# Optimization experiments

Hardware: AMD Instinct MI355X
Metric: run time of the kernel (lower is better)

## Reference

```python
import jax, jax.numpy as jnp
import numpy as np

EPS = 1e-5

def layer_norm(x, g, b):
    m = jnp.mean(x, axis=-1, keepdims=True)
    v = jnp.var(x, axis=-1, keepdims=True)
    return (x - m) / jnp.sqrt(v + EPS) * g + b

def setup_inputs() -> dict:
    key = jax.random.key(0)
    B, N, D, H, F = 2, 2048, 1024, 16, 4096
    ks = jax.random.split(key, 12)
    s = 0.02
    return {
        "x": jax.random.normal(ks[0], (B, N, D), dtype=jnp.float32),
        "wq": jax.random.normal(ks[1], (D, D), dtype=jnp.float32) * s,
        "bq": jnp.zeros((D,), jnp.float32),
        "wk": jax.random.normal(ks[2], (D, D), dtype=jnp.float32) * s,
        "bk": jnp.zeros((D,), jnp.float32),
        "wv": jax.random.normal(ks[3], (D, D), dtype=jnp.float32) * s,
        "bv": jnp.zeros((D,), jnp.float32),
        "g1": jnp.ones((D,), jnp.float32),
        "b1": jnp.zeros((D,), jnp.float32),
        "g2": jnp.ones((D,), jnp.float32),
        "b2": jnp.zeros((D,), jnp.float32),
        "w1": jax.random.normal(ks[4], (D, F), dtype=jnp.float32) * s,
        "bw1": jnp.zeros((F,), jnp.float32),
        "gf": jnp.ones((F,), jnp.float32),
        "bf": jnp.zeros((F,), jnp.float32),
        "w2": jax.random.normal(ks[5], (F, D), dtype=jnp.float32) * s,
        "bw2": jnp.zeros((D,), jnp.float32),
        "num_heads": 16,
    }

def reference(x, wq, bq, wk, bk, wv, bv, g1, b1, g2, b2, w1, bw1, gf, bf, w2, bw2, num_heads):
    B, N, D = x.shape
    H = num_heads
    E = D // H
    h = layer_norm(x, g1, b1)
    q = (h @ wq + bq).reshape(B, N, H, E).transpose(0, 2, 1, 3)  # B H N E
    k = (h @ wk + bk).reshape(B, N, H, E).transpose(0, 2, 1, 3)
    v = (h @ wv + bv).reshape(B, N, H, E).transpose(0, 2, 1, 3)
    # NOTE: original scales by 1/sqrt(1/emb_dim) == sqrt(emb_dim)
    scale = jnp.sqrt(jnp.float32(D))
    score = jnp.einsum('bhne,bhme->bhnm', q, k) * scale  # B H N N
    w = jax.nn.softmax(score, axis=-1)
    attn = jnp.einsum('bhnm,bhme->bhne', w, v)
    attn = attn.transpose(0, 2, 1, 3).reshape(B, N, D)
    x = x + attn  # dropout = identity in eval
    h2 = layer_norm(x, g2, b2)
    # MLP: Linear -> (Dropout) -> LayerNorm -> ReLU -> Linear; NO residual add (faithful to source)
    u = layer_norm(h2 @ w1 + bw1, gf, bf)
    return jax.nn.relu(u) @ w2 + bw2
```

## Files before the change

kernel.cpp:

```cpp
#include <hip/hip_runtime.h>

typedef unsigned short u16;
typedef _Float16 f16;
typedef _Float16 f16x8 __attribute__((ext_vector_type(8)));
typedef float f32x4 __attribute__((ext_vector_type(4)));
typedef unsigned short u16x4 __attribute__((ext_vector_type(4)));
typedef unsigned int u32x4 __attribute__((ext_vector_type(4)));

__device__ __forceinline__ u16 f2h(float f) {
    f16 h = (f16)f;
    return *reinterpret_cast<u16*>(&h);
}
__device__ __forceinline__ float h2f(u16 u) {
    f16 h = *reinterpret_cast<f16*>(&u);
    return (float)h;
}

__device__ __forceinline__ unsigned cvtpkh(float lo, float hi) {
    unsigned r;
    asm volatile("v_cvt_pkrtz_f16_f32 %0, %1, %2" : "=v"(r) : "v"(lo), "v"(hi));
    return r;
}

__device__ __forceinline__ void gload16(const u16* g, u16* l) {
    __builtin_amdgcn_global_load_lds((const __attribute__((address_space(1))) unsigned int*)g,
                                     (__attribute__((address_space(3))) unsigned int*)l, 16, 0, 0);
}

__global__ void transpose_cast3(const float* __restrict__ W0, u16* __restrict__ T0,
                                const float* __restrict__ W1, u16* __restrict__ T1,
                                const float* __restrict__ W2, u16* __restrict__ T2,
                                int K, int N) {
    __shared__ float t[32][33];
    const float* W = (blockIdx.z == 0) ? W0 : (blockIdx.z == 1) ? W1 : W2;
    u16* Wt = (blockIdx.z == 0) ? T0 : (blockIdx.z == 1) ? T1 : T2;
    const int n0 = blockIdx.x * 32, k0 = blockIdx.y * 32;
    const int tx = threadIdx.x, ty = threadIdx.y;
#pragma unroll
    for (int i = 0; i < 32; i += 8)
        t[ty + i][tx] = W[(size_t)(k0 + ty + i) * N + n0 + tx];
    __syncthreads();
#pragma unroll
    for (int i = 0; i < 32; i += 8)
        Wt[(size_t)(n0 + ty + i) * K + k0 + tx] = f2h(t[tx][ty + i]);
}

__global__ void transpose_cast(const float* __restrict__ W, u16* __restrict__ Wt,
                               int K, int N) {
    __shared__ float t[32][33];
    const int n0 = blockIdx.x * 32, k0 = blockIdx.y * 32;
    const int tx = threadIdx.x, ty = threadIdx.y;
#pragma unroll
    for (int i = 0; i < 32; i += 8)
        t[ty + i][tx] = W[(size_t)(k0 + ty + i) * N + n0 + tx];
    __syncthreads();
#pragma unroll
    for (int i = 0; i < 32; i += 8)
        Wt[(size_t)(n0 + ty + i) * K + k0 + tx] = f2h(t[tx][ty + i]);
}

__global__ __launch_bounds__(256) void ln_f32_f16(const float* __restrict__ in,
                                                  const float* __restrict__ g,
                                                  const float* __restrict__ b,
                                                  u16* __restrict__ out) {
    constexpr int Dl = 1024;
    const int row = blockIdx.x, tid = threadIdx.x;
    const float4 v = *(const float4*)&in[(size_t)row * Dl + tid * 4];
    const float* vp = (const float*)&v;
    float s = v.x + v.y + v.z + v.w;
    float s2 = v.x * v.x + v.y * v.y + v.z * v.z + v.w * v.w;
#pragma unroll
    for (int off = 32; off; off >>= 1) { s += __shfl_xor(s, off); s2 += __shfl_xor(s2, off); }
    __shared__ float red[8];
    const int lane = tid & 63, wid = tid >> 6;
    if (lane == 0) { red[wid] = s; red[4 + wid] = s2; }
    __syncthreads();
    s = red[0] + red[1] + red[2] + red[3];
    s2 = red[4] + red[5] + red[6] + red[7];
    const float mean = s * (1.0f / Dl);
    const float rstd = rsqrtf(s2 * (1.0f / Dl) - mean * mean + 1e-5f);
    u16x4 pk;
#pragma unroll
    for (int i = 0; i < 4; ++i) {
        const int col = tid * 4 + i;
        pk[i] = f2h((vp[i] - mean) * rstd * g[col] + b[col]);
    }
    *(u16x4*)&out[(size_t)row * Dl + tid * 4] = pk;
}

__global__ __launch_bounds__(256) void ln_relu_f16(u16* __restrict__ mid,
                                                   const float* __restrict__ g,
                                                   const float* __restrict__ b) {
    constexpr int Fl = 4096;
    const int row = blockIdx.x, tid = threadIdx.x;
    u16* rp = mid + (size_t)row * Fl;
    float v[16];
    u32x4 raw[2];
#pragma unroll
    for (int c = 0; c < 2; ++c) raw[c] = *(const u32x4*)&rp[tid * 16 + c * 8];
#pragma unroll
    for (int c = 0; c < 2; ++c)
#pragma unroll
        for (int j = 0; j < 4; ++j) {
            const unsigned u = raw[c][j];
            v[c * 8 + j * 2] = h2f((u16)(u & 0xffffu));
            v[c * 8 + j * 2 + 1] = h2f((u16)(u >> 16));
        }
    float s = 0.f, s2 = 0.f;
#pragma unroll
    for (int i = 0; i < 16; ++i) { s += v[i]; s2 += v[i] * v[i]; }
#pragma unroll
    for (int off = 32; off; off >>= 1) { s += __shfl_xor(s, off); s2 += __shfl_xor(s2, off); }
    __shared__ float red[8];
    const int lane = tid & 63, wid = tid >> 6;
    if (lane == 0) { red[wid] = s; red[4 + wid] = s2; }
    __syncthreads();
    s = red[0] + red[1] + red[2] + red[3];
    s2 = red[4] + red[5] + red[6] + red[7];
    const float mean = s * (1.0f / Fl);
    const float rstd = rsqrtf(s2 * (1.0f / Fl) - mean * mean + 1e-5f);
    unsigned w[8];
#pragma unroll
    for (int j = 0; j < 8; ++j) {
        const int col = tid * 16 + j * 2;
        const float y0 = fmaxf((v[j * 2] - mean) * rstd * g[col] + b[col], 0.f);
        const float y1 = fmaxf((v[j * 2 + 1] - mean) * rstd * g[col + 1] + b[col + 1], 0.f);
        w[j] = (unsigned)f2h(y0) | ((unsigned)f2h(y1) << 16);
    }
    *(u32x4*)&rp[tid * 16] = *(u32x4*)&w[0];
    *(u32x4*)&rp[tid * 16 + 8] = *(u32x4*)&w[4];
}

template <int EPI, int BN>
__global__ __launch_bounds__(256, 2) void gemm_f16(const u16* __restrict__ A,
                                                   const u16* __restrict__ Bt,
                                                   const float* __restrict__ bias,
                                                   u16* __restrict__ outB,
                                                   float* __restrict__ outF,
                                                   int M_, int N_, int K_) {
    constexpr int BK = 32;
    constexpr int NJ = BN / 32;
    __shared__ u16 As[128 * BK];
    __shared__ u16 Bs[BN * BK];
    const int tid = threadIdx.x;
    const int lane = tid & 63;
    const int wid = tid >> 6;
    const int m0 = blockIdx.y * 128;
    const int n0 = blockIdx.x * BN;
    const int wr = (wid >> 1) * 64;
    const int wc = (wid & 1) * (BN / 2);
    const int fr = lane & 15;
    const int fg = (lane >> 4) * 8;

    const int srow = wid * 32 + (lane >> 2);
    const int srB = wid * (BN / 4) + (lane >> 2);
    const int scol = (lane & 3) * 8;
    const u16* pa0 = A + (size_t)(m0 + srow) * K_ + scol;
    const u16* pa1 = pa0 + (size_t)16 * K_;
    const u16* pb0 = Bt + (size_t)(n0 + srB) * K_ + scol;
    const u16* pb1 = pb0 + (size_t)16 * K_;
    u16* lA0 = As + wid * 1024;
    u16* lA1 = lA0 + 512;
    u16* lB0 = Bs + wid * (BN / 4) * BK;
    u16* lB1 = lB0 + 512;

    f32x4 acc[4][NJ] = {};

    for (int k0 = 0; k0 < K_; k0 += BK) {
        __syncthreads();
        gload16(pa0, lA0); gload16(pa1, lA1);
        gload16(pb0, lB0);
        if constexpr (BN == 128) gload16(pb1, lB1);
        pa0 += BK; pa1 += BK; pb0 += BK; pb1 += BK;
        __syncthreads();
        f16x8 aF[4], bF[NJ];
#pragma unroll
        for (int i = 0; i < 4; ++i) aF[i] = *(const f16x8*)&As[(wr + i * 16 + fr) * BK + fg];
#pragma unroll
        for (int j = 0; j < NJ; ++j) bF[j] = *(const f16x8*)&Bs[(wc + j * 16 + fr) * BK + fg];
#pragma unroll
        for (int i = 0; i < 4; ++i)
#pragma unroll
            for (int j = 0; j < NJ; ++j)
                acc[i][j] = __builtin_amdgcn_mfma_f32_16x16x32_f16(aF[i], bF[j], acc[i][j], 0, 0, 0);
    }

    const int g4 = (lane >> 4) * 4;
#pragma unroll
    for (int i = 0; i < 4; ++i) {
#pragma unroll
        for (int j = 0; j < NJ; ++j) {
            const int mb = m0 + wr + i * 16 + g4;
            const int nb = n0 + wc + j * 16 + fr;
            const float bv = bias[nb];
            if constexpr (EPI == 0) {
#pragma unroll
                for (int r = 0; r < 4; ++r)
                    outB[(size_t)(mb + r) * N_ + nb] = f2h(acc[i][j][r] + bv);
            } else {
#pragma unroll
                for (int r = 0; r < 4; ++r)
                    outF[(size_t)(mb + r) * N_ + nb] = acc[i][j][r] + bv;
            }
        }
    }
}

__global__ __launch_bounds__(256, 4) void gemm_qkv(const u16* __restrict__ A,
                                                   const u16* __restrict__ qW,
                                                   const u16* __restrict__ kW,
                                                   const u16* __restrict__ vW,
                                                   const float* __restrict__ bq,
                                                   const float* __restrict__ bk,
                                                   const float* __restrict__ bv,
                                                   u16* __restrict__ qb, u16* __restrict__ kb,
                                                   u16* __restrict__ vtb,
                                                   int M_, int K_) {
    constexpr int BK = 32;
    __shared__ u16 As[128 * BK];
    __shared__ u16 Bs[64 * BK];
    const int tid = threadIdx.x;
    const int lane = tid & 63;
    const int wid = tid >> 6;
    const int region = blockIdx.x >> 4;
    const int n0 = (blockIdx.x & 15) * 64;
    const int m0 = blockIdx.y * 128;
    const int wr = (wid >> 1) * 64;
    const int wc = (wid & 1) * 32;
    const int fr = lane & 15;
    const int fg = (lane >> 4) * 8;

    const int srow = wid * 32 + (lane >> 2);
    const int srB = wid * 16 + (lane >> 2);
    const int scol = (lane & 3) * 8;

    const u16* B = (region == 0) ? qW : (region == 1) ? kW : vW;
    const u16* pa0 = A + (size_t)(m0 + srow) * K_ + scol;
    const u16* pa1 = pa0 + (size_t)16 * K_;
    const u16* pb = B + (size_t)(n0 + srB) * K_ + scol;
    u16* lA0 = As + wid * 1024;
    u16* lA1 = lA0 + 512;
    u16* lB = Bs + wid * 512;

    f32x4 acc[4][2] = {};

    for (int k0 = 0; k0 < K_; k0 += BK) {
        __syncthreads();
        gload16(pa0, lA0); gload16(pa1, lA1);
        gload16(pb, lB);
        pa0 += BK; pa1 += BK; pb += BK;
        __syncthreads();
        f16x8 aF[4], bF[2];
#pragma unroll
        for (int i = 0; i < 4; ++i) aF[i] = *(const f16x8*)&As[(wr + i * 16 + fr) * BK + fg];
#pragma unroll
        for (int j = 0; j < 2; ++j) bF[j] = *(const f16x8*)&Bs[(wc + j * 16 + fr) * BK + fg];
#pragma unroll
        for (int i = 0; i < 4; ++i)
#pragma unroll
            for (int j = 0; j < 2; ++j)
                acc[i][j] = __builtin_amdgcn_mfma_f32_16x16x32_f16(aF[i], bF[j], acc[i][j], 0, 0, 0);
    }

    const float* bias = (region == 0) ? bq : (region == 1) ? bk : bv;
    const float scale = (region == 0) ? 32.f : 1.f;
    const int g4 = (lane >> 4) * 4;
#pragma unroll
    for (int i = 0; i < 4; ++i) {
#pragma unroll
        for (int j = 0; j < 2; ++j) {
            const int mb = m0 + wr + i * 16 + g4;
            const int nb = n0 + wc + j * 16 + fr;
            const float bv_ = bias[nb];
            const int h = nb >> 6, e = nb & 63;
            if (region < 2) {
                u16* outp = (region == 0) ? qb : kb;
#pragma unroll
                for (int r = 0; r < 4; ++r) {
                    const int m = mb + r;
                    const size_t idx = ((size_t)((m >> 11) * 16 + h) * 2048 + (m & 2047)) * 64 + e;
                    outp[idx] = f2h((acc[i][j][r] + bv_) * scale);
                }
            } else {
                const int b_ = mb >> 11, np = mb & 2047;
                u16x4 pk;
#pragma unroll
                for (int r = 0; r < 4; ++r) pk[r] = f2h(acc[i][j][r] + bv_);
                *(u16x4*)&vtb[((size_t)(b_ * 16 + h) * 64 + e) * 2048 + np] = pk;
            }
        }
    }
}

__global__ __launch_bounds__(512, 4) void attn_kernel(const u16* __restrict__ q,
                                                      const u16* __restrict__ k,
                                                      const u16* __restrict__ vt,
                                                      const float* __restrict__ x,
                                                      float* __restrict__ x2) {
    constexpr int N = 2048, E = 64, KB = 64, NT = N / KB;
    constexpr float L2E = 1.4426950408889634f;
    __shared__ u16 Ks[2][64 * 64];
    __shared__ u16 Vs[2][64 * 64];
    __shared__ unsigned Ps[8][16][36];

    const int tid = threadIdx.x;
    const int lane = tid & 63;
    const int wid = tid >> 6;
    const int bh = blockIdx.x >> 4;
    const int q0 = (blockIdx.x & 15) * 128;
    const u16* qh = q + (size_t)bh * N * E;
    const u16* kh = k + (size_t)bh * N * E;
    const u16* vh = vt + (size_t)bh * E * N;

    const int fr = lane & 15;
    const int fgrp = lane >> 4;
    const int fg8 = fgrp * 8;
    int pc[2];
#pragma unroll
    for (int ks = 0; ks < 2; ++ks) pc[ks] = 8 * (((ks << 2) + fgrp) ^ (fr & 7));

    const int srow = wid * 8 + (lane >> 3);
    const int swc = 8 * ((lane & 7) ^ (lane >> 3));
    u16* dK = &Ks[0][wid * 8 * 64];
    u16* dV = &Vs[0][wid * 8 * 64];
    constexpr int BUFO = 64 * 64;

    f16x8 qf[2];
#pragma unroll
    for (int ks = 0; ks < 2; ++ks)
        qf[ks] = *(const f16x8*)&qh[(size_t)(q0 + wid * 16 + fr) * E + ks * 32 + fg8];

    auto stage = [&](int t, int buf) {
        const size_t kb = (size_t)t * KB;
        gload16(kh + (kb + srow) * E + swc, dK + buf * BUFO);
        gload16(vh + (size_t)srow * N + kb + swc, dV + buf * BUFO);
    };

    f32x4 o[4] = {};
    float mrow = -1e30f, lpart = 0.f;

    stage(0, 0);

    for (int t = 0; t < NT; ++t) {
        const int buf = t & 1;
        __syncthreads();
        if (t + 1 < NT) {
            stage(t + 1, buf ^ 1);
            asm volatile("s_waitcnt vmcnt(2)" ::: "memory");
        } else {
            asm volatile("s_waitcnt vmcnt(0)" ::: "memory");
        }
        __syncthreads();

        const u16* KK = &Ks[buf][0];
        const u16* VV = &Vs[buf][0];

        f32x4 s[4] = {};
#pragma unroll
        for (int fn = 0; fn < 4; ++fn)
#pragma unroll
            for (int ks = 0; ks < 2; ++ks) {
                const f16x8 kf = *(const f16x8*)&KK[(fn * 16 + fr) * 64 + pc[ks]];
                s[fn] = __builtin_amdgcn_mfma_f32_16x16x32_f16(kf, qf[ks], s[fn], 0, 0, 0);
            }

        float lmax = fmaxf(fmaxf(fmaxf(s[0][0], s[0][1]), fmaxf(s[0][2], s[0][3])),
                           fmaxf(fmaxf(s[1][0], s[1][1]), fmaxf(s[1][2], s[1][3])));
        lmax = fmaxf(lmax, fmaxf(fmaxf(fmaxf(s[2][0], s[2][1]), fmaxf(s[2][2], s[2][3])),
                                 fmaxf(fmaxf(s[3][0], s[3][1]), fmaxf(s[3][2], s[3][3]))));
        if (!__all(lmax <= mrow + 8.f)) {
            float m2 = fmaxf(lmax, __shfl_xor(lmax, 16));
            m2 = fmaxf(m2, __shfl_xor(m2, 32));
            const float mnew = fmaxf(mrow, m2);
            const float fac = exp2f((mrow - mnew) * L2E);
            mrow = mnew;
            lpart *= fac;
            float fo[4];
#pragma unroll
            for (int r = 0; r < 4; ++r) fo[r] = __shfl(fac, fgrp * 4 + r);
#pragma unroll
            for (int fe = 0; fe < 4; ++fe)
#pragma unroll
                for (int r = 0; r < 4; ++r) o[fe][r] *= fo[r];
        }

        const float nml = -mrow * L2E;
#pragma unroll
        for (int fn = 0; fn < 4; ++fn) {
            const float p0 = exp2f(fmaf(s[fn][0], L2E, nml));
            const float p1 = exp2f(fmaf(s[fn][1], L2E, nml));
            const float p2 = exp2f(fmaf(s[fn][2], L2E, nml));
            const float p3 = exp2f(fmaf(s[fn][3], L2E, nml));
            lpart += (p0 + p1) + (p2 + p3);
            uint2 w;
            w.x = cvtpkh(p0, p1);
            w.y = cvtpkh(p2, p3);
            *(uint2*)&Ps[wid][fr][fn * 8 + fgrp * 2] = w;
        }

        const u16* prow = (const u16*)&Ps[wid][fr][0];
        f16x8 pf[2];
#pragma unroll
        for (int ks = 0; ks < 2; ++ks) pf[ks] = *(const f16x8*)&prow[ks * 32 + fg8];
#pragma unroll
        for (int fe = 0; fe < 4; ++fe)
#pragma unroll
            for (int ks = 0; ks < 2; ++ks) {
                const f16x8 vf = *(const f16x8*)&VV[(fe * 16 + fr) * 64 + pc[ks]];
                o[fe] = __builtin_amdgcn_mfma_f32_16x16x32_f16(pf[ks], vf, o[fe], 0, 0, 0);
            }
    }

    float lsum = lpart + __shfl_xor(lpart, 16);
    lsum += __shfl_xor(lsum, 32);
    float rl[4];
#pragma unroll
    for (int r = 0; r < 4; ++r) rl[r] = 1.0f / __shfl(lsum, fgrp * 4 + r);

    const int b_ = bh >> 4, h_ = bh & 15;
#pragma unroll
    for (int fe = 0; fe < 4; ++fe)
#pragma unroll
        for (int r = 0; r < 4; ++r) {
            const int npos = q0 + wid * 16 + fgrp * 4 + r;
            const size_t idx = ((size_t)(b_ * 2048 + npos)) * 1024 + h_ * 64 + fe * 16 + fr;
            x2[idx] = x[idx] + o[fe][r] * rl[r];
        }
}

extern "C" void kernel_launch(void* const* d_in, const int* in_sizes, int n_in,
                              void* d_out, int out_size, void* d_ws, size_t ws_size,
                              hipStream_t stream) {
    const float* x = (const float*)d_in[0];
    const float* wq = (const float*)d_in[1];
    const float* bq = (const float*)d_in[2];
    const float* wk = (const float*)d_in[3];
    const float* bk = (const float*)d_in[4];
    const float* wv = (const float*)d_in[5];
    const float* bv = (const float*)d_in[6];
    const float* g1 = (const float*)d_in[7];
    const float* b1 = (const float*)d_in[8];
    const float* g2 = (const float*)d_in[9];
    const float* b2 = (const float*)d_in[10];
    const float* w1 = (const float*)d_in[11];
    const float* bw1 = (const float*)d_in[12];
    const float* gf = (const float*)d_in[13];
    const float* bf = (const float*)d_in[14];
    const float* w2 = (const float*)d_in[15];
    const float* bw2 = (const float*)d_in[16];
    float* out = (float*)d_out;

    constexpr int Bc = 2, Nc = 2048, Dc = 1024, Fc = 4096, Mc = 4096;

    char* ws = (char*)d_ws;
    auto alloc = [&](size_t bytes) {
        char* p = ws;
        ws += (bytes + 255) & ~(size_t)255;
        return p;
    };
    u16* wqt = (u16*)alloc((size_t)Dc * Dc * 2);
    u16* wkt = (u16*)alloc((size_t)Dc * Dc * 2);
    u16* wvt = (u16*)alloc((size_t)Dc * Dc * 2);
    u16* w1t = (u16*)alloc((size_t)Dc * Fc * 2);
    u16* w2t = (u16*)alloc((size_t)Fc * Dc * 2);
    char* region = (char*)alloc((size_t)Mc * Dc * 2 * 4);
    u16* h1 = (u16*)region;
    u16* qb = h1 + (size_t)Mc * Dc;
    u16* kb = qb + (size_t)Mc * Dc;
    u16* vtb = kb + (size_t)Mc * Dc;
    u16* mid = (u16*)region;
    float* x2 = (float*)alloc((size_t)Mc * Dc * 4);
    u16* h2 = (u16*)alloc((size_t)Mc * Dc * 2);

    const dim3 tb(32, 8);
    transpose_cast3<<<dim3(Dc / 32, Dc / 32, 3), tb, 0, stream>>>(wq, wqt, wk, wkt, wv, wvt, Dc, Dc);
    transpose_cast<<<dim3(Fc / 32, Dc / 32), tb, 0, stream>>>(w1, w1t, Dc, Fc);
    transpose_cast<<<dim3(Dc / 32, Fc / 32), tb, 0, stream>>>(w2, w2t, Fc, Dc);

    ln_f32_f16<<<Mc, 256, 0, stream>>>(x, g1, b1, h1);

    gemm_qkv<<<dim3(48, Mc / 128), 256, 0, stream>>>(h1, wqt, wkt, wvt, bq, bk, bv,
                                                     qb, kb, vtb, Mc, Dc);

    attn_kernel<<<Bc * 16 * (Nc / 128), 512, 0, stream>>>(qb, kb, vtb, x, x2);

    ln_f32_f16<<<Mc, 256, 0, stream>>>(x2, g2, b2, h2);

    gemm_f16<0, 128><<<dim3(Fc / 128, Mc / 128), 256, 0, stream>>>(h2, w1t, bw1, mid, nullptr, Mc, Fc, Dc);

    ln_relu_f16<<<Mc, 256, 0, stream>>>(mid, gf, bf);

    gemm_f16<1, 64><<<dim3(Dc / 64, Mc / 128), 256, 0, stream>>>(mid, w2t, bw2, nullptr, out, Mc, Dc, Fc);
}
```

Baseline: 283.5 us.

## Double-buffer LDS in GEMM kernels and use raw barriers in attention loop

The GEMM and QKV GEMM main loops now use two LDS buffers, issuing the global-to-LDS load for the next K tile before the MFMAs on the current tile, with one vmcnt(0) wait and one barrier per iteration instead of two syncthreads. This aims to hide global load latency behind compute. The attention loop replaces __syncthreads with raw s_barrier, which may remove the compiler-inserted lgkmcnt waits. The risks are a doubled LDS footprint per block, which can lower occupancy, and weaker memory ordering from the raw barriers.

```diff
diff --git a/kernel.cpp b/kernel.cpp
--- a/kernel.cpp
+++ b/kernel.cpp
@@ -26,6 +26,9 @@
     __builtin_amdgcn_global_load_lds((const __attribute__((address_space(1))) unsigned int*)g,
                                      (__attribute__((address_space(3))) unsigned int*)l, 16, 0, 0);
 }
+
+#define RAW_BARRIER() __builtin_amdgcn_s_barrier()
+#define WAITCNT_VM(N) asm volatile("s_waitcnt vmcnt(" #N ")" ::: "memory")
 
 __global__ void transpose_cast3(const float* __restrict__ W0, u16* __restrict__ T0,
                                 const float* __restrict__ W1, u16* __restrict__ T1,
@@ -140,8 +143,8 @@
                                                    int M_, int N_, int K_) {
     constexpr int BK = 32;
     constexpr int NJ = BN / 32;
-    __shared__ u16 As[128 * BK];
-    __shared__ u16 Bs[BN * BK];
+    __shared__ u16 As[2][128 * BK];
+    __shared__ u16 Bs[2][BN * BK];
     const int tid = threadIdx.x;
     const int lane = tid & 63;
     const int wid = tid >> 6;
@@ -159,30 +162,38 @@
     const u16* pa1 = pa0 + (size_t)16 * K_;
     const u16* pb0 = Bt + (size_t)(n0 + srB) * K_ + scol;
     const u16* pb1 = pb0 + (size_t)16 * K_;
-    u16* lA0 = As + wid * 1024;
-    u16* lA1 = lA0 + 512;
-    u16* lB0 = Bs + wid * (BN / 4) * BK;
-    u16* lB1 = lB0 + 512;
+    const int aoff = wid * 1024;
+    const int boff = wid * (BN / 4) * BK;
+
+    auto stage = [&](int k0, int buf) {
+        gload16(pa0 + k0, &As[buf][aoff]);
+        gload16(pa1 + k0, &As[buf][aoff + 512]);
+        gload16(pb0 + k0, &Bs[buf][boff]);
+        if constexpr (BN == 128) gload16(pb1 + k0, &Bs[buf][boff + 512]);
+    };
 
     f32x4 acc[4][NJ] = {};
-
-    for (int k0 = 0; k0 < K_; k0 += BK) {
-        __syncthreads();
-        gload16(pa0, lA0); gload16(pa1, lA1);
-        gload16(pb0, lB0);
-        if constexpr (BN == 128) gload16(pb1, lB1);
-        pa0 += BK; pa1 += BK; pb0 += BK; pb1 += BK;
-        __syncthreads();
+    const int nt = K_ / BK;
+
+    stage(0, 0);
+    WAITCNT_VM(0);
+    RAW_BARRIER();
+
+    for (int t = 0; t < nt; ++t) {
+        const int buf = t & 1;
+        if (t + 1 < nt) stage((t + 1) * BK, buf ^ 1);
         f16x8 aF[4], bF[NJ];
 #pragma unroll
-        for (int i = 0; i < 4; ++i) aF[i] = *(const f16x8*)&As[(wr + i * 16 + fr) * BK + fg];
-#pragma unroll
-        for (int j = 0; j < NJ; ++j) bF[j] = *(const f16x8*)&Bs[(wc + j * 16 + fr) * BK + fg];
+        for (int i = 0; i < 4; ++i) aF[i] = *(const f16x8*)&As[buf][(wr + i * 16 + fr) * BK + fg];
+#pragma unroll
+        for (int j = 0; j < NJ; ++j) bF[j] = *(const f16x8*)&Bs[buf][(wc + j * 16 + fr) * BK + fg];
 #pragma unroll
         for (int i = 0; i < 4; ++i)
 #pragma unroll
             for (int j = 0; j < NJ; ++j)
                 acc[i][j] = __builtin_amdgcn_mfma_f32_16x16x32_f16(aF[i], bF[j], acc[i][j], 0, 0, 0);
+        WAITCNT_VM(0);
+        RAW_BARRIER();
     }
 
     const int g4 = (lane >> 4) * 4;
@@ -217,8 +228,8 @@
                                                    u16* __restrict__ vtb,
                                                    int M_, int K_) {
     constexpr int BK = 32;
-    __shared__ u16 As[128 * BK];
-    __shared__ u16 Bs[64 * BK];
+    __shared__ u16 As[2][128 * BK];
+    __shared__ u16 Bs[2][64 * BK];
     const int tid = threadIdx.x;
     const int lane = tid & 63;
     const int wid = tid >> 6;
@@ -238,28 +249,37 @@
     const u16* pa0 = A + (size_t)(m0 + srow) * K_ + scol;
     const u16* pa1 = pa0 + (size_t)16 * K_;
     const u16* pb = B + (size_t)(n0 + srB) * K_ + scol;
-    u16* lA0 = As + wid * 1024;
-    u16* lA1 = lA0 + 512;
-    u16* lB = Bs + wid * 512;
+    const int aoff = wid * 1024;
+    const int boff = wid * 512;
+
+    auto stage = [&](int k0, int buf) {
+        gload16(pa0 + k0, &As[buf][aoff]);
+        gload16(pa1 + k0, &As[buf][aoff + 512]);
+        gload16(pb + k0, &Bs[buf][boff]);
+    };
 
     f32x4 acc[4][2] = {};
-
-    for (int k0 = 0; k0 < K_; k0 += BK) {
-        __syncthreads();
-        gload16(pa0, lA0); gload16(pa1, lA1);
-        gload16(pb, lB);
-        pa0 += BK; pa1 += BK; pb += BK;
-        __syncthreads();
+    const int nt = K_ / BK;
+
+    stage(0, 0);
+    WAITCNT_VM(0);
+    RAW_BARRIER();
+
+    for (int t = 0; t < nt; ++t) {
+        const int buf = t & 1;
+        if (t + 1 < nt) stage((t + 1) * BK, buf ^ 1);
         f16x8 aF[4], bF[2];
 #pragma unroll
-        for (int i = 0; i < 4; ++i) aF[i] = *(const f16x8*)&As[(wr + i * 16 + fr) * BK + fg];
-#pragma unroll
-        for (int j = 0; j < 2; ++j) bF[j] = *(const f16x8*)&Bs[(wc + j * 16 + fr) * BK + fg];
+        for (int i = 0; i < 4; ++i) aF[i] = *(const f16x8*)&As[buf][(wr + i * 16 + fr) * BK + fg];
+#pragma unroll
+        for (int j = 0; j < 2; ++j) bF[j] = *(const f16x8*)&Bs[buf][(wc + j * 16 + fr) * BK + fg];
 #pragma unroll
         for (int i = 0; i < 4; ++i)
 #pragma unroll
             for (int j = 0; j < 2; ++j)
                 acc[i][j] = __builtin_amdgcn_mfma_f32_16x16x32_f16(aF[i], bF[j], acc[i][j], 0, 0, 0);
+        WAITCNT_VM(0);
+        RAW_BARRIER();
     }
 
     const float* bias = (region == 0) ? bq : (region == 1) ? bk : bv;
@@ -343,14 +363,14 @@
 
     for (int t = 0; t < NT; ++t) {
         const int buf = t & 1;
-        __syncthreads();
+        RAW_BARRIER();
         if (t + 1 < NT) {
             stage(t + 1, buf ^ 1);
-            asm volatile("s_waitcnt vmcnt(2)" ::: "memory");
+            WAITCNT_VM(2);
         } else {
-            asm volatile("s_waitcnt vmcnt(0)" ::: "memory");
-        }
-        __syncthreads();
+            WAITCNT_VM(0);
+        }
+        RAW_BARRIER();
 
         const u16* KK = &Ks[buf][0];
         const u16* VV = &Vs[buf][0];
```

Result: no change. 287.1 us (+1.2%).
